# Performance work log

Hardware: AMD Instinct MI355X
Metric: run time of the kernel (lower is better)

The kernel has to match this reference:

```python
import jax, jax.numpy as jnp
import numpy as np

NUM_EMBEDDINGS = 512
EMBEDDING_DIM = 64
COMMITMENT_COST = 0.25


def setup_inputs() -> dict:
    key = jax.random.key(0)
    k1, k2 = jax.random.split(key)
    inputs = jax.random.normal(k1, (32, 4096, EMBEDDING_DIM), dtype=jnp.float32)
    # original init: uniform(-1/K, 1/K)
    weight = jax.random.uniform(
        k2, (NUM_EMBEDDINGS, EMBEDDING_DIM), dtype=jnp.float32,
        minval=-1.0 / NUM_EMBEDDINGS, maxval=1.0 / NUM_EMBEDDINGS)
    return {"inputs": inputs, "weight": weight, "is_training": 1}


def reference(inputs, weight, is_training):
    input_shape = inputs.shape
    flat = inputs.reshape(-1, EMBEDDING_DIM)                      # [N, D]
    distances = (jnp.sum(flat ** 2, axis=1, keepdims=True)
                 + jnp.sum(weight ** 2, axis=1)
                 - 2.0 * flat @ weight.T)                         # [N, K]
    encoding_indices = jnp.argmin(distances, axis=1)              # [N]
    # one-hot @ codebook == direct gather
    quantized = weight[encoding_indices].reshape(input_shape)

    sg = jax.lax.stop_gradient
    e_latent_loss = jnp.mean((sg(quantized) - inputs) ** 2)
    q_latent_loss = jnp.mean((quantized - sg(inputs)) ** 2)
    loss = q_latent_loss + COMMITMENT_COST * e_latent_loss

    quantized_st = inputs + sg(quantized - inputs)                # straight-through

    n = encoding_indices.shape[0]
    counts = jnp.zeros(NUM_EMBEDDINGS, dtype=jnp.float32).at[encoding_indices].add(1.0)
    avg_probs = counts / n
    perplexity = jnp.exp(-jnp.sum(avg_probs * jnp.log(avg_probs + 1e-10)))

    encoding_indices_show = encoding_indices.reshape(1, -1)
    return loss, quantized_st, perplexity, encoding_indices_show
```

## Files before the change

kernel.cpp:

```cpp
#include <hip/hip_runtime.h>

#define N_ROWS 131072
#define DIM 64
#define KCODES 512
#define MARGIN 1e-4f
#define QCAP 16384

typedef __attribute__((ext_vector_type(8))) short bf16x8;
typedef __attribute__((ext_vector_type(4))) float f32x4;


__device__ __forceinline__ float sqr_nf(float x) {
    float s = x * x;
    asm("" : "+v"(s));
    return s;
}

__device__ __forceinline__ unsigned short f2bf(float f) {
    unsigned u = __float_as_uint(f);
    u += 0x7fffu + ((u >> 16) & 1u);
    return (unsigned short)(u >> 16);
}
__device__ __forceinline__ float bf2f(unsigned short b) {
    return __uint_as_float(((unsigned)b) << 16);
}

__device__ __forceinline__ void cvtpair(float4 a, float4 b, bf16x8& hi, bf16x8& lo) {
    float v[8] = {a.x, a.y, a.z, a.w, b.x, b.y, b.z, b.w};
#pragma unroll
    for (int j = 0; j < 8; ++j) {
        unsigned short h = f2bf(v[j]);
        hi[j] = (short)h;
        lo[j] = (short)f2bf(v[j] - bf2f(h));
    }
}
__device__ __forceinline__ float4 scl(float4 v, float s) {
    return make_float4(v.x * s, v.y * s, v.z * s, v.w * s);
}

__global__ __launch_bounds__(256) void vq_wprep_k(
    const float* __restrict__ W, unsigned short* __restrict__ wfrag,
    float* __restrict__ bnp) {
    int code = blockIdx.x * 256 + threadIdx.x;
    float p[64];
#pragma unroll
    for (int i = 0; i < 16; ++i) {
        float4 v = reinterpret_cast<const float4*>(W)[code * 16 + i];
        p[i * 4 + 0] = v.x; p[i * 4 + 1] = v.y;
        p[i * 4 + 2] = v.z; p[i * 4 + 3] = v.w;
    }
    unsigned short hi[64], lo[64];
#pragma unroll
    for (int d = 0; d < 64; ++d) {
        hi[d] = f2bf(p[d]);
        lo[d] = f2bf(p[d] - bf2f(hi[d]));
    }
    {
        float r[8];
#pragma unroll
        for (int j = 0; j < 8; ++j) r[j] = sqr_nf(p[j]);
#pragma unroll
        for (int i = 1; i < 8; ++i)
#pragma unroll
            for (int j = 0; j < 8; ++j) r[j] += sqr_nf(p[i * 8 + j]);
        bnp[code] = ((r[0] + r[1]) + (r[2] + r[3])) + ((r[4] + r[5]) + (r[6] + r[7]));
    }
    const int cti = code >> 4, m = code & 15;
#pragma unroll
    for (int part = 0; part < 2; ++part) {
        const unsigned short* src = part ? lo : hi;
#pragma unroll
        for (int s = 0; s < 2; ++s) {
            int q = part * 2 + s;
#pragma unroll
            for (int kq = 0; kq < 4; ++kq) {
                int lane = kq * 16 + m;
                size_t off = ((size_t)(cti * 4 + q) * 64 + lane) * 8;
                *reinterpret_cast<uint4*>(wfrag + off) =
                    *reinterpret_cast<const uint4*>(src + s * 32 + kq * 8);
            }
        }
    }
}

__global__ __launch_bounds__(256, 4) void vq_score_k(
    const float* __restrict__ X, const unsigned short* __restrict__ wfrag,
    const float* __restrict__ bnp, float* __restrict__ out_idx) {
    const int tid = threadIdx.x;
    const int lane = tid & 63, w = tid >> 6;
    const int m = lane & 15, kq = lane >> 4;
    const long rbase = (long)blockIdx.x * 128;

    bf16x8 ahi[2][2], alo[2][2];
#pragma unroll
    for (int rt = 0; rt < 2; ++rt) {
        long row = rbase + w * 32 + rt * 16 + m;
        const float4* xp = reinterpret_cast<const float4*>(X + row * DIM);
        cvtpair(scl(xp[kq * 2], -2.f), scl(xp[kq * 2 + 1], -2.f),
                ahi[rt][0], alo[rt][0]);
        cvtpair(scl(xp[8 + kq * 2], -2.f), scl(xp[8 + kq * 2 + 1], -2.f),
                ahi[rt][1], alo[rt][1]);
    }

    float best[2][4], sec[2][4];
    int bidx[2][4];
#pragma unroll
    for (int rt = 0; rt < 2; ++rt)
#pragma unroll
        for (int j = 0; j < 4; ++j) { best[rt][j] = 3e38f; sec[rt][j] = 3e38f; bidx[rt][j] = 0; }

    const bf16x8* fb = reinterpret_cast<const bf16x8*>(wfrag);
    bf16x8 nb0 = fb[lane], nb1 = fb[64 + lane], nb2 = fb[128 + lane], nb3 = fb[192 + lane];
    for (int cti = 0; cti < 32; ++cti) {
        bf16x8 b0 = nb0, b1 = nb1, b2 = nb2, b3 = nb3;
        if (cti < 31) {
            int nbase = (cti + 1) * 256;
            nb0 = fb[nbase + lane];       nb1 = fb[nbase + 64 + lane];
            nb2 = fb[nbase + 128 + lane]; nb3 = fb[nbase + 192 + lane];
        }
        const int kk = cti * 16 + m;
        const float wn = bnp[kk];
        f32x4 c0 = {wn, wn, wn, wn};
        f32x4 c1 = {wn, wn, wn, wn};
        c0 = __builtin_amdgcn_mfma_f32_16x16x32_bf16(ahi[0][0], b0, c0, 0, 0, 0);
        c1 = __builtin_amdgcn_mfma_f32_16x16x32_bf16(ahi[1][0], b0, c1, 0, 0, 0);
        c0 = __builtin_amdgcn_mfma_f32_16x16x32_bf16(ahi[0][1], b1, c0, 0, 0, 0);
        c1 = __builtin_amdgcn_mfma_f32_16x16x32_bf16(ahi[1][1], b1, c1, 0, 0, 0);
        c0 = __builtin_amdgcn_mfma_f32_16x16x32_bf16(alo[0][0], b0, c0, 0, 0, 0);
        c1 = __builtin_amdgcn_mfma_f32_16x16x32_bf16(alo[1][0], b0, c1, 0, 0, 0);
        c0 = __builtin_amdgcn_mfma_f32_16x16x32_bf16(alo[0][1], b1, c0, 0, 0, 0);
        c1 = __builtin_amdgcn_mfma_f32_16x16x32_bf16(alo[1][1], b1, c1, 0, 0, 0);
        c0 = __builtin_amdgcn_mfma_f32_16x16x32_bf16(ahi[0][0], b2, c0, 0, 0, 0);
        c1 = __builtin_amdgcn_mfma_f32_16x16x32_bf16(ahi[1][0], b2, c1, 0, 0, 0);
        c0 = __builtin_amdgcn_mfma_f32_16x16x32_bf16(ahi[0][1], b3, c0, 0, 0, 0);
        c1 = __builtin_amdgcn_mfma_f32_16x16x32_bf16(ahi[1][1], b3, c1, 0, 0, 0);
#pragma unroll
        for (int rt = 0; rt < 2; ++rt)
#pragma unroll
            for (int j = 0; j < 4; ++j) {
                float s = (rt == 0) ? c0[j] : c1[j];
                float nb = fminf(best[rt][j], s);
                float ns = fminf(sec[rt][j], fmaxf(best[rt][j], s));
                bidx[rt][j] = (s < best[rt][j]) ? kk : bidx[rt][j];
                best[rt][j] = nb; sec[rt][j] = ns;
            }
    }

#pragma unroll
    for (int st = 1; st < 16; st <<= 1) {
#pragma unroll
        for (int rt = 0; rt < 2; ++rt)
#pragma unroll
            for (int j = 0; j < 4; ++j) {
                float ob = __shfl_xor(best[rt][j], st);
                float os = __shfl_xor(sec[rt][j], st);
                int oi = __shfl_xor(bidx[rt][j], st);
                if (ob < best[rt][j] || (ob == best[rt][j] && oi < bidx[rt][j])) {
                    sec[rt][j] = fminf(best[rt][j], os);
                    best[rt][j] = ob; bidx[rt][j] = oi;
                } else {
                    sec[rt][j] = fminf(sec[rt][j], ob);
                }
            }
    }

    if (m == 0) {
#pragma unroll
        for (int rt = 0; rt < 2; ++rt)
#pragma unroll
            for (int j = 0; j < 4; ++j) {
                int r = w * 32 + rt * 16 + kq * 4 + j;
                int id = (sec[rt][j] - best[rt][j] <= MARGIN) ? -1 : bidx[rt][j];
                out_idx[rbase + r] = (float)id;
            }
    }
}

__global__ __launch_bounds__(256, 4) void vq_post_k(
    const float* __restrict__ X, const float* __restrict__ Wf,
    const float* __restrict__ bnp,
    float* __restrict__ out_q, float* __restrict__ out_idx,
    unsigned* __restrict__ hist8, float* __restrict__ lossp,
    unsigned* __restrict__ qcount, unsigned* __restrict__ queue) {
    const int tid = threadIdx.x;
    const int lane = tid & 63, w = tid >> 6;
    const int g = lane >> 4, l16 = lane & 15;
    const long wbase = ((long)blockIdx.x * 4 + w) * 32;
    const unsigned hstripe = (blockIdx.x & 7) * KCODES;

    float idxv = (lane < 32) ? out_idx[wbase + lane] : 1.0f;

    int mypos = -1;
    if (lane < 32 && idxv < 0.f) {
        mypos = (int)atomicAdd(qcount, 1u);
        if (mypos < QCAP) queue[mypos] = (unsigned)(wbase + lane);
    }

    float4 xv[8], wv[8];
    int kk[8];
#pragma unroll
    for (int i = 0; i < 8; ++i) {
        int r = g * 8 + i;
        float kf = __shfl(idxv, r);
        kk[i] = (kf >= 0.f) ? (int)kf : -1;
        xv[i] = reinterpret_cast<const float4*>(X)[(wbase + r) * 16 + l16];
        int ksafe = (kk[i] >= 0) ? kk[i] : 0;
        wv[i] = reinterpret_cast<const float4*>(Wf)[(long)ksafe * 16 + l16];
    }

    float ls = 0.f;
#pragma unroll
    for (int i = 0; i < 8; ++i) {
        if (kk[i] >= 0) {
            float4 o; float t;
            t = wv[i].x - xv[i].x; o.x = xv[i].x + t; ls = fmaf(t, t, ls);
            t = wv[i].y - xv[i].y; o.y = xv[i].y + t; ls = fmaf(t, t, ls);
            t = wv[i].z - xv[i].z; o.z = xv[i].z + t; ls = fmaf(t, t, ls);
            t = wv[i].w - xv[i].w; o.w = xv[i].w + t; ls = fmaf(t, t, ls);
            reinterpret_cast<float4*>(out_q)[(wbase + g * 8 + i) * 16 + l16] = o;
            if (l16 == 0) atomicAdd(&hist8[hstripe + kk[i]], 1u);
        }
    }

    unsigned long long inl = __ballot(mypos >= QCAP);
    while (inl) {
        const int b = __ffsll((long long)inl) - 1;
        inl &= inl - 1;
        const long rrow = wbase + b;
        const float xvv = X[rrow * DIM + lane];
        float sq = sqr_nf(xvv);
        float rr = sq;
#pragma unroll
        for (int t2 = 1; t2 < 8; ++t2) rr += __shfl(sq, (lane & 7) + 8 * t2);
        float t01 = rr + __shfl_xor(rr, 1);
        float t03 = t01 + __shfl_xor(t01, 2);
        float Afull = t03 + __shfl_xor(t03, 4);
        const float A = __shfl(Afull, 0);
        float acc[8];
#pragma unroll
        for (int c = 0; c < 8; ++c) acc[c] = 0.f;
        for (int d0 = 0; d0 < 16; ++d0) {
            float x0 = __shfl(xvv, d0 * 4 + 0);
            float x1 = __shfl(xvv, d0 * 4 + 1);
            float x2 = __shfl(xvv, d0 * 4 + 2);
            float x3 = __shfl(xvv, d0 * 4 + 3);
#pragma unroll
            for (int c = 0; c < 8; ++c) {
                float4 wq = *reinterpret_cast<const float4*>(
                    &Wf[(lane * 8 + c) * DIM + d0 * 4]);
                acc[c] = fmaf(x0, wq.x, acc[c]);
                acc[c] = fmaf(x1, wq.y, acc[c]);
                acc[c] = fmaf(x2, wq.z, acc[c]);
                acc[c] = fmaf(x3, wq.w, acc[c]);
            }
        }
        float bs = 3e38f;
        int bi = 0;
#pragma unroll
        for (int c = 0; c < 8; ++c) {
            int kkk = lane * 8 + c;
            float u = A + bnp[kkk];
            float s2 = u - 2.0f * acc[c];
            if (s2 < bs) { bs = s2; bi = kkk; }
        }
#pragma unroll
        for (int st = 1; st < 64; st <<= 1) {
            float ob = __shfl_xor(bs, st);
            int oi = __shfl_xor(bi, st);
            if (ob < bs || (ob == bs && oi < bi)) { bs = ob; bi = oi; }
        }
        const int k = bi;
        if (lane == 0) {
            out_idx[rrow] = (float)k;
            atomicAdd(&hist8[hstripe + k], 1u);
        }
        float qv = Wf[k * DIM + lane];
        float diff = qv - xvv;
        out_q[rrow * DIM + lane] = xvv + diff;
        ls = fmaf(diff, diff, ls);
    }

#pragma unroll
    for (int st = 1; st < 64; st <<= 1) ls += __shfl_xor(ls, st);
    if (lane == 0 && ls != 0.f) atomicAdd(&lossp[blockIdx.x & 255], ls);
}

#define WTP 516
__global__ __launch_bounds__(1024) void vq_refine_k(
    const float* __restrict__ X, const float* __restrict__ Wf,
    const float* __restrict__ bnp,
    float* __restrict__ out_q, float* __restrict__ out_idx,
    unsigned* __restrict__ hist8, float* __restrict__ lossp,
    const unsigned* __restrict__ qcount, const unsigned* __restrict__ queue) {
    __shared__ float WT[64 * WTP];
    const int tid = threadIdx.x;
    const int lane = tid & 63, wv = tid >> 6;

#pragma unroll
    for (int i = 0; i < 8; ++i) {
        int f = i * 1024 + tid;
        int k = f >> 4, c4 = f & 15;
        float4 v = reinterpret_cast<const float4*>(Wf)[f];
        WT[(c4 * 4 + 0) * WTP + k] = v.x;
        WT[(c4 * 4 + 1) * WTP + k] = v.y;
        WT[(c4 * 4 + 2) * WTP + k] = v.z;
        WT[(c4 * 4 + 3) * WTP + k] = v.w;
    }
    __syncthreads();

    unsigned n = *qcount;
    if (n > QCAP) n = QCAP;
    const int gwave = blockIdx.x * 16 + wv;

    float ls = 0.f;
    for (unsigned j = gwave; j < n; j += 256 * 16) {
        const long row = (long)queue[j];
        const float xv = X[row * DIM + lane];
        float sq = sqr_nf(xv);
        float rr = sq;
#pragma unroll
        for (int t2 = 1; t2 < 8; ++t2) rr += __shfl(sq, (lane & 7) + 8 * t2);
        float t01 = rr + __shfl_xor(rr, 1);
        float t03 = t01 + __shfl_xor(t01, 2);
        float Afull = t03 + __shfl_xor(t03, 4);
        const float A = __shfl(Afull, 0);
        float acc[8];
#pragma unroll
        for (int c = 0; c < 8; ++c) acc[c] = 0.f;
        for (int d = 0; d < 64; ++d) {
            float xd = __shfl(xv, d);
#pragma unroll
            for (int c = 0; c < 8; ++c)
                acc[c] = fmaf(xd, WT[d * WTP + c * 64 + lane], acc[c]);
        }
        float bs = 3e38f;
        int bi = 0;
#pragma unroll
        for (int c = 0; c < 8; ++c) {
            int k = c * 64 + lane;
            float u = A + bnp[k];
            float s2 = u - 2.0f * acc[c];
            if (s2 < bs) { bs = s2; bi = k; }
        }
#pragma unroll
        for (int st = 1; st < 64; st <<= 1) {
            float ob = __shfl_xor(bs, st);
            int oi = __shfl_xor(bi, st);
            if (ob < bs || (ob == bs && oi < bi)) { bs = ob; bi = oi; }
        }
        const int k = bi;
        if (lane == 0) {
            out_idx[row] = (float)k;
            atomicAdd(&hist8[(j & 7) * KCODES + k], 1u);
        }
        float qv = WT[lane * WTP + k];
        float diff = qv - xv;
        out_q[row * DIM + lane] = xv + diff;
        ls = fmaf(diff, diff, ls);
    }

#pragma unroll
    for (int st = 1; st < 64; st <<= 1) ls += __shfl_xor(ls, st);
    if (lane == 0 && ls != 0.f) atomicAdd(&lossp[gwave & 255], ls);
}

__global__ __launch_bounds__(512) void vq_finalize_k(
    const unsigned* __restrict__ hist8, const float* __restrict__ lossp,
    float* __restrict__ out_loss, float* __restrict__ out_perp) {
    __shared__ float red[512];
    int t = threadIdx.x;
    unsigned c = 0;
#pragma unroll
    for (int s = 0; s < 8; ++s) c += hist8[s * KCODES + t];
    float p = (float)c * (1.0f / (float)N_ROWS);
    red[t] = p * logf(p + 1e-10f);
    __syncthreads();
    for (int off = 256; off; off >>= 1) {
        if (t < off) red[t] += red[t + off];
        __syncthreads();
    }
    if (t == 0) *out_perp = expf(-red[0]);
    __syncthreads();
    red[t] = (t < 256) ? lossp[t] : 0.f;
    __syncthreads();
    for (int off = 256; off; off >>= 1) {
        if (t < off) red[t] += red[t + off];
        __syncthreads();
    }
    if (t == 0) {
        float m = red[0] / (float)(N_ROWS * DIM);
        *out_loss = m + 0.25f * m;
    }
}

extern "C" void kernel_launch(void* const* d_in, const int* in_sizes, int n_in,
                              void* d_out, int out_size, void* d_ws, size_t ws_size,
                              hipStream_t stream) {
    const float* X = (const float*)d_in[0];
    const float* Wf = (const float*)d_in[1];

    float* out = (float*)d_out;
    float* out_loss = out;
    float* out_q = out + 1;
    float* out_perp = out + 1 + (long)N_ROWS * DIM;
    float* out_idx = out + 2 + (long)N_ROWS * DIM;

    unsigned* wsu = (unsigned*)d_ws;
    float* lossp = (float*)d_ws;
    unsigned* hist8 = wsu + 256;
    unsigned* qcount = wsu + 4352;
    unsigned* queue = wsu + 4360;
    float* bnp = (float*)(wsu + 20744);
    unsigned short* wfrag = (unsigned short*)(wsu + 21256);

    hipMemsetAsync(d_ws, 0, 17412, stream);
    vq_wprep_k<<<2, 256, 0, stream>>>(Wf, wfrag, bnp);
    vq_score_k<<<N_ROWS / 128, 256, 0, stream>>>(X, wfrag, bnp, out_idx);
    vq_post_k<<<N_ROWS / 128, 256, 0, stream>>>(X, Wf, bnp, out_q, out_idx,
                                                hist8, lossp, qcount, queue);
    vq_refine_k<<<256, 1024, 0, stream>>>(X, Wf, bnp, out_q, out_idx,
                                          hist8, lossp, qcount, queue);
    vq_finalize_k<<<1, 512, 0, stream>>>(hist8, lossp, out_loss, out_perp);
}
```

Baseline: 110.4 us.

## Halve rows per wave in score kernel and split MFMA accumulators into independent chains

The score kernel now handles 16 rows per wave instead of 32, which doubles the grid and raises the launch-bounds occupancy hint from 4 to 6. The six MFMAs per code tile are spread across three independent accumulators (hi*hi, lo*hi, hi*lo) that are summed at the end, instead of two long dependent chains. This aims to cut register pressure, raise occupancy and shorten MFMA dependency chains. In exchange, each codebook fragment loaded is reused across half as many rows, and the extra vector adds may change rounding of the scores slightly.

```diff
diff --git a/kernel.cpp b/kernel.cpp
--- a/kernel.cpp
+++ b/kernel.cpp
@@ -83,31 +83,26 @@
     }
 }
 
-__global__ __launch_bounds__(256, 4) void vq_score_k(
+__global__ __launch_bounds__(256, 6) void vq_score_k(
     const float* __restrict__ X, const unsigned short* __restrict__ wfrag,
     const float* __restrict__ bnp, float* __restrict__ out_idx) {
     const int tid = threadIdx.x;
     const int lane = tid & 63, w = tid >> 6;
     const int m = lane & 15, kq = lane >> 4;
-    const long rbase = (long)blockIdx.x * 128;
-
-    bf16x8 ahi[2][2], alo[2][2];
-#pragma unroll
-    for (int rt = 0; rt < 2; ++rt) {
-        long row = rbase + w * 32 + rt * 16 + m;
+    const long rbase = (long)blockIdx.x * 64;
+
+    bf16x8 ahi[2], alo[2];
+    {
+        long row = rbase + w * 16 + m;
         const float4* xp = reinterpret_cast<const float4*>(X + row * DIM);
-        cvtpair(scl(xp[kq * 2], -2.f), scl(xp[kq * 2 + 1], -2.f),
-                ahi[rt][0], alo[rt][0]);
-        cvtpair(scl(xp[8 + kq * 2], -2.f), scl(xp[8 + kq * 2 + 1], -2.f),
-                ahi[rt][1], alo[rt][1]);
-    }
-
-    float best[2][4], sec[2][4];
-    int bidx[2][4];
-#pragma unroll
-    for (int rt = 0; rt < 2; ++rt)
-#pragma unroll
-        for (int j = 0; j < 4; ++j) { best[rt][j] = 3e38f; sec[rt][j] = 3e38f; bidx[rt][j] = 0; }
+        cvtpair(scl(xp[kq * 2], -2.f), scl(xp[kq * 2 + 1], -2.f), ahi[0], alo[0]);
+        cvtpair(scl(xp[8 + kq * 2], -2.f), scl(xp[8 + kq * 2 + 1], -2.f), ahi[1], alo[1]);
+    }
+
+    float best[4], sec[4];
+    int bidx[4];
+#pragma unroll
+    for (int j = 0; j < 4; ++j) { best[j] = 3e38f; sec[j] = 3e38f; bidx[j] = 0; }
 
     const bf16x8* fb = reinterpret_cast<const bf16x8*>(wfrag);
     bf16x8 nb0 = fb[lane], nb1 = fb[64 + lane], nb2 = fb[128 + lane], nb3 = fb[192 + lane];
@@ -120,59 +115,49 @@
         }
         const int kk = cti * 16 + m;
         const float wn = bnp[kk];
-        f32x4 c0 = {wn, wn, wn, wn};
-        f32x4 c1 = {wn, wn, wn, wn};
-        c0 = __builtin_amdgcn_mfma_f32_16x16x32_bf16(ahi[0][0], b0, c0, 0, 0, 0);
-        c1 = __builtin_amdgcn_mfma_f32_16x16x32_bf16(ahi[1][0], b0, c1, 0, 0, 0);
-        c0 = __builtin_amdgcn_mfma_f32_16x16x32_bf16(ahi[0][1], b1, c0, 0, 0, 0);
-        c1 = __builtin_amdgcn_mfma_f32_16x16x32_bf16(ahi[1][1], b1, c1, 0, 0, 0);
-        c0 = __builtin_amdgcn_mfma_f32_16x16x32_bf16(alo[0][0], b0, c0, 0, 0, 0);
-        c1 = __builtin_amdgcn_mfma_f32_16x16x32_bf16(alo[1][0], b0, c1, 0, 0, 0);
-        c0 = __builtin_amdgcn_mfma_f32_16x16x32_bf16(alo[0][1], b1, c0, 0, 0, 0);
-        c1 = __builtin_amdgcn_mfma_f32_16x16x32_bf16(alo[1][1], b1, c1, 0, 0, 0);
-        c0 = __builtin_amdgcn_mfma_f32_16x16x32_bf16(ahi[0][0], b2, c0, 0, 0, 0);
-        c1 = __builtin_amdgcn_mfma_f32_16x16x32_bf16(ahi[1][0], b2, c1, 0, 0, 0);
-        c0 = __builtin_amdgcn_mfma_f32_16x16x32_bf16(ahi[0][1], b3, c0, 0, 0, 0);
-        c1 = __builtin_amdgcn_mfma_f32_16x16x32_bf16(ahi[1][1], b3, c1, 0, 0, 0);
-#pragma unroll
-        for (int rt = 0; rt < 2; ++rt)
-#pragma unroll
-            for (int j = 0; j < 4; ++j) {
-                float s = (rt == 0) ? c0[j] : c1[j];
-                float nb = fminf(best[rt][j], s);
-                float ns = fminf(sec[rt][j], fmaxf(best[rt][j], s));
-                bidx[rt][j] = (s < best[rt][j]) ? kk : bidx[rt][j];
-                best[rt][j] = nb; sec[rt][j] = ns;
+        f32x4 chh = {wn, wn, wn, wn};
+        f32x4 clh = {0.f, 0.f, 0.f, 0.f};
+        f32x4 chl = {0.f, 0.f, 0.f, 0.f};
+        chh = __builtin_amdgcn_mfma_f32_16x16x32_bf16(ahi[0], b0, chh, 0, 0, 0);
+        clh = __builtin_amdgcn_mfma_f32_16x16x32_bf16(alo[0], b0, clh, 0, 0, 0);
+        chl = __builtin_amdgcn_mfma_f32_16x16x32_bf16(ahi[0], b2, chl, 0, 0, 0);
+        chh = __builtin_amdgcn_mfma_f32_16x16x32_bf16(ahi[1], b1, chh, 0, 0, 0);
+        clh = __builtin_amdgcn_mfma_f32_16x16x32_bf16(alo[1], b1, clh, 0, 0, 0);
+        chl = __builtin_amdgcn_mfma_f32_16x16x32_bf16(ahi[1], b3, chl, 0, 0, 0);
+        f32x4 acc = (chh + clh) + chl;
+#pragma unroll
+        for (int j = 0; j < 4; ++j) {
+            float s = acc[j];
+            float nb = fminf(best[j], s);
+            float ns = fminf(sec[j], fmaxf(best[j], s));
+            bidx[j] = (s < best[j]) ? kk : bidx[j];
+            best[j] = nb; sec[j] = ns;
+        }
+    }
+
+#pragma unroll
+    for (int st = 1; st < 16; st <<= 1) {
+#pragma unroll
+        for (int j = 0; j < 4; ++j) {
+            float ob = __shfl_xor(best[j], st);
+            float os = __shfl_xor(sec[j], st);
+            int oi = __shfl_xor(bidx[j], st);
+            if (ob < best[j] || (ob == best[j] && oi < bidx[j])) {
+                sec[j] = fminf(best[j], os);
+                best[j] = ob; bidx[j] = oi;
+            } else {
+                sec[j] = fminf(sec[j], ob);
             }
-    }
-
-#pragma unroll
-    for (int st = 1; st < 16; st <<= 1) {
-#pragma unroll
-        for (int rt = 0; rt < 2; ++rt)
-#pragma unroll
-            for (int j = 0; j < 4; ++j) {
-                float ob = __shfl_xor(best[rt][j], st);
-                float os = __shfl_xor(sec[rt][j], st);
-                int oi = __shfl_xor(bidx[rt][j], st);
-                if (ob < best[rt][j] || (ob == best[rt][j] && oi < bidx[rt][j])) {
-                    sec[rt][j] = fminf(best[rt][j], os);
-                    best[rt][j] = ob; bidx[rt][j] = oi;
-                } else {
-                    sec[rt][j] = fminf(sec[rt][j], ob);
-                }
-            }
+        }
     }
 
     if (m == 0) {
 #pragma unroll
-        for (int rt = 0; rt < 2; ++rt)
-#pragma unroll
-            for (int j = 0; j < 4; ++j) {
-                int r = w * 32 + rt * 16 + kq * 4 + j;
-                int id = (sec[rt][j] - best[rt][j] <= MARGIN) ? -1 : bidx[rt][j];
-                out_idx[rbase + r] = (float)id;
-            }
+        for (int j = 0; j < 4; ++j) {
+            int r = w * 16 + kq * 4 + j;
+            int id = (sec[j] - best[j] <= MARGIN) ? -1 : bidx[j];
+            out_idx[rbase + r] = (float)id;
+        }
     }
 }
 
@@ -415,7 +400,7 @@
 
     hipMemsetAsync(d_ws, 0, 17412, stream);
     vq_wprep_k<<<2, 256, 0, stream>>>(Wf, wfrag, bnp);
-    vq_score_k<<<N_ROWS / 128, 256, 0, stream>>>(X, wfrag, bnp, out_idx);
+    vq_score_k<<<N_ROWS / 64, 256, 0, stream>>>(X, wfrag, bnp, out_idx);
     vq_post_k<<<N_ROWS / 128, 256, 0, stream>>>(X, Wf, bnp, out_q, out_idx,
                                                 hist8, lossp, qcount, queue);
     vq_refine_k<<<256, 1024, 0, stream>>>(X, Wf, bnp, out_q, out_idx,
```

Result: slower. 117.5 us (+6.5%).

## Double-buffer codebook fragment prefetch and stage code norms in shared memory

Applied to the files above, without the earlier changes.

The codebook fragment loads move from a one-tile-ahead prefetch to two interleaved register buffers that run two tiles ahead, hiding more global-load latency. Code norms are staged into LDS once per block instead of being read from global memory every iteration. MFMA chains are reordered per row tile into two independent accumulators (c0 and c1) that are summed afterwards, which shortens the dependent MFMA chain. The cost is more live registers for the second prefetch buffer, a block-wide barrier, and a changed summation order that may perturb near-tie argmin results.

```diff
diff --git a/kernel.cpp b/kernel.cpp
--- a/kernel.cpp
+++ b/kernel.cpp
@@ -83,13 +83,43 @@
     }
 }
 
+#define SCORE_STEP(CTI, B0, B1, B2, B3)                                           \
+    {                                                                             \
+        const int kk = (CTI) * 16 + m;                                            \
+        const float wn = bnp_s[kk];                                               \
+        _Pragma("unroll")                                                         \
+        for (int rt = 0; rt < 2; ++rt) {                                          \
+            f32x4 c0 = {wn, wn, wn, wn};                                          \
+            f32x4 c1 = {0.f, 0.f, 0.f, 0.f};                                      \
+            c0 = __builtin_amdgcn_mfma_f32_16x16x32_bf16(ahi[rt][0], B0, c0, 0, 0, 0); \
+            c1 = __builtin_amdgcn_mfma_f32_16x16x32_bf16(ahi[rt][0], B2, c1, 0, 0, 0); \
+            c0 = __builtin_amdgcn_mfma_f32_16x16x32_bf16(alo[rt][0], B0, c0, 0, 0, 0); \
+            c1 = __builtin_amdgcn_mfma_f32_16x16x32_bf16(ahi[rt][1], B3, c1, 0, 0, 0); \
+            c0 = __builtin_amdgcn_mfma_f32_16x16x32_bf16(ahi[rt][1], B1, c0, 0, 0, 0); \
+            c0 = __builtin_amdgcn_mfma_f32_16x16x32_bf16(alo[rt][1], B1, c0, 0, 0, 0); \
+            f32x4 acc = c0 + c1;                                                  \
+            _Pragma("unroll")                                                     \
+            for (int j = 0; j < 4; ++j) {                                         \
+                float s = acc[j];                                                 \
+                float nb = fminf(best[rt][j], s);                                 \
+                float ns = fminf(sec[rt][j], fmaxf(best[rt][j], s));              \
+                bidx[rt][j] = (s < best[rt][j]) ? kk : bidx[rt][j];               \
+                best[rt][j] = nb; sec[rt][j] = ns;                                \
+            }                                                                     \
+        }                                                                         \
+    }
+
 __global__ __launch_bounds__(256, 4) void vq_score_k(
     const float* __restrict__ X, const unsigned short* __restrict__ wfrag,
     const float* __restrict__ bnp, float* __restrict__ out_idx) {
+    __shared__ float bnp_s[KCODES];
     const int tid = threadIdx.x;
     const int lane = tid & 63, w = tid >> 6;
     const int m = lane & 15, kq = lane >> 4;
     const long rbase = (long)blockIdx.x * 128;
+
+    bnp_s[tid] = bnp[tid];
+    bnp_s[256 + tid] = bnp[256 + tid];
 
     bf16x8 ahi[2][2], alo[2][2];
 #pragma unroll
@@ -101,6 +131,7 @@
         cvtpair(scl(xp[8 + kq * 2], -2.f), scl(xp[8 + kq * 2 + 1], -2.f),
                 ahi[rt][1], alo[rt][1]);
     }
+    __syncthreads();
 
     float best[2][4], sec[2][4];
     int bidx[2][4];
@@ -110,40 +141,28 @@
         for (int j = 0; j < 4; ++j) { best[rt][j] = 3e38f; sec[rt][j] = 3e38f; bidx[rt][j] = 0; }
 
     const bf16x8* fb = reinterpret_cast<const bf16x8*>(wfrag);
-    bf16x8 nb0 = fb[lane], nb1 = fb[64 + lane], nb2 = fb[128 + lane], nb3 = fb[192 + lane];
-    for (int cti = 0; cti < 32; ++cti) {
-        bf16x8 b0 = nb0, b1 = nb1, b2 = nb2, b3 = nb3;
-        if (cti < 31) {
-            int nbase = (cti + 1) * 256;
-            nb0 = fb[nbase + lane];       nb1 = fb[nbase + 64 + lane];
-            nb2 = fb[nbase + 128 + lane]; nb3 = fb[nbase + 192 + lane];
-        }
-        const int kk = cti * 16 + m;
-        const float wn = bnp[kk];
-        f32x4 c0 = {wn, wn, wn, wn};
-        f32x4 c1 = {wn, wn, wn, wn};
-        c0 = __builtin_amdgcn_mfma_f32_16x16x32_bf16(ahi[0][0], b0, c0, 0, 0, 0);
-        c1 = __builtin_amdgcn_mfma_f32_16x16x32_bf16(ahi[1][0], b0, c1, 0, 0, 0);
-        c0 = __builtin_amdgcn_mfma_f32_16x16x32_bf16(ahi[0][1], b1, c0, 0, 0, 0);
-        c1 = __builtin_amdgcn_mfma_f32_16x16x32_bf16(ahi[1][1], b1, c1, 0, 0, 0);
-        c0 = __builtin_amdgcn_mfma_f32_16x16x32_bf16(alo[0][0], b0, c0, 0, 0, 0);
-        c1 = __builtin_amdgcn_mfma_f32_16x16x32_bf16(alo[1][0], b0, c1, 0, 0, 0);
-        c0 = __builtin_amdgcn_mfma_f32_16x16x32_bf16(alo[0][1], b1, c0, 0, 0, 0);
-        c1 = __builtin_amdgcn_mfma_f32_16x16x32_bf16(alo[1][1], b1, c1, 0, 0, 0);
-        c0 = __builtin_amdgcn_mfma_f32_16x16x32_bf16(ahi[0][0], b2, c0, 0, 0, 0);
-        c1 = __builtin_amdgcn_mfma_f32_16x16x32_bf16(ahi[1][0], b2, c1, 0, 0, 0);
-        c0 = __builtin_amdgcn_mfma_f32_16x16x32_bf16(ahi[0][1], b3, c0, 0, 0, 0);
-        c1 = __builtin_amdgcn_mfma_f32_16x16x32_bf16(ahi[1][1], b3, c1, 0, 0, 0);
-#pragma unroll
-        for (int rt = 0; rt < 2; ++rt)
-#pragma unroll
-            for (int j = 0; j < 4; ++j) {
-                float s = (rt == 0) ? c0[j] : c1[j];
-                float nb = fminf(best[rt][j], s);
-                float ns = fminf(sec[rt][j], fmaxf(best[rt][j], s));
-                bidx[rt][j] = (s < best[rt][j]) ? kk : bidx[rt][j];
-                best[rt][j] = nb; sec[rt][j] = ns;
-            }
+    bf16x8 pa0 = fb[lane], pa1 = fb[64 + lane], pa2 = fb[128 + lane], pa3 = fb[192 + lane];
+    bf16x8 pb0 = fb[256 + lane], pb1 = fb[320 + lane], pb2 = fb[384 + lane], pb3 = fb[448 + lane];
+
+    for (int cti = 0; cti < 32; cti += 2) {
+        {
+            bf16x8 b0 = pa0, b1 = pa1, b2 = pa2, b3 = pa3;
+            if (cti + 2 < 32) {
+                int nb = (cti + 2) * 256;
+                pa0 = fb[nb + lane];       pa1 = fb[nb + 64 + lane];
+                pa2 = fb[nb + 128 + lane]; pa3 = fb[nb + 192 + lane];
+            }
+            SCORE_STEP(cti, b0, b1, b2, b3);
+        }
+        {
+            bf16x8 b0 = pb0, b1 = pb1, b2 = pb2, b3 = pb3;
+            if (cti + 3 < 32) {
+                int nb = (cti + 3) * 256;
+                pb0 = fb[nb + lane];       pb1 = fb[nb + 64 + lane];
+                pb2 = fb[nb + 128 + lane]; pb3 = fb[nb + 192 + lane];
+            }
+            SCORE_STEP(cti + 1, b0, b1, b2, b3);
+        }
     }
 
 #pragma unroll
```

Result: slower. 148.2 us (+34.3%).

## Stage codebook fragments in LDS with 1024-thread score blocks

Applied to the files above, without the earlier changes.

The score kernel now uses 1024-thread blocks, each covering 512 rows. It copies the whole 128 KB bf16 codebook fragment array and the codeword norms into shared memory once per block, so the inner loop reads B operands from LDS rather than global/L2. The MFMA chain is also reordered into two independent accumulators per row tile, which are summed afterwards to shorten the dependency chain. In exchange, 128 KB of LDS per block caps occupancy at one block per CU, and launch_bounds(1024,4) may be unattainable and put pressure on registers.

```diff
diff --git a/kernel.cpp b/kernel.cpp
--- a/kernel.cpp
+++ b/kernel.cpp
@@ -83,13 +83,23 @@
     }
 }
 
-__global__ __launch_bounds__(256, 4) void vq_score_k(
+__global__ __launch_bounds__(1024, 4) void vq_score_k(
     const float* __restrict__ X, const unsigned short* __restrict__ wfrag,
     const float* __restrict__ bnp, float* __restrict__ out_idx) {
+    __shared__ __align__(16) unsigned short Wlds[65536];
+    __shared__ float bnp_s[KCODES];
     const int tid = threadIdx.x;
     const int lane = tid & 63, w = tid >> 6;
     const int m = lane & 15, kq = lane >> 4;
-    const long rbase = (long)blockIdx.x * 128;
+    const long rbase = (long)blockIdx.x * 512;
+
+    {
+        const uint4* g = reinterpret_cast<const uint4*>(wfrag);
+        uint4* l4 = reinterpret_cast<uint4*>(Wlds);
+#pragma unroll
+        for (int i = 0; i < 8; ++i) l4[i * 1024 + tid] = g[i * 1024 + tid];
+    }
+    if (tid < KCODES) bnp_s[tid] = bnp[tid];
 
     bf16x8 ahi[2][2], alo[2][2];
 #pragma unroll
@@ -101,6 +111,7 @@
         cvtpair(scl(xp[8 + kq * 2], -2.f), scl(xp[8 + kq * 2 + 1], -2.f),
                 ahi[rt][1], alo[rt][1]);
     }
+    __syncthreads();
 
     float best[2][4], sec[2][4];
     int bidx[2][4];
@@ -109,41 +120,37 @@
 #pragma unroll
         for (int j = 0; j < 4; ++j) { best[rt][j] = 3e38f; sec[rt][j] = 3e38f; bidx[rt][j] = 0; }
 
-    const bf16x8* fb = reinterpret_cast<const bf16x8*>(wfrag);
-    bf16x8 nb0 = fb[lane], nb1 = fb[64 + lane], nb2 = fb[128 + lane], nb3 = fb[192 + lane];
+    const bf16x8* fp = reinterpret_cast<const bf16x8*>(Wlds);
+    bf16x8 nb0 = fp[lane], nb1 = fp[64 + lane], nb2 = fp[128 + lane], nb3 = fp[192 + lane];
     for (int cti = 0; cti < 32; ++cti) {
         bf16x8 b0 = nb0, b1 = nb1, b2 = nb2, b3 = nb3;
         if (cti < 31) {
-            int nbase = (cti + 1) * 256;
-            nb0 = fb[nbase + lane];       nb1 = fb[nbase + 64 + lane];
-            nb2 = fb[nbase + 128 + lane]; nb3 = fb[nbase + 192 + lane];
+            int nbi = (cti + 1) * 256;
+            nb0 = fp[nbi + lane];       nb1 = fp[nbi + 64 + lane];
+            nb2 = fp[nbi + 128 + lane]; nb3 = fp[nbi + 192 + lane];
         }
         const int kk = cti * 16 + m;
-        const float wn = bnp[kk];
-        f32x4 c0 = {wn, wn, wn, wn};
-        f32x4 c1 = {wn, wn, wn, wn};
-        c0 = __builtin_amdgcn_mfma_f32_16x16x32_bf16(ahi[0][0], b0, c0, 0, 0, 0);
-        c1 = __builtin_amdgcn_mfma_f32_16x16x32_bf16(ahi[1][0], b0, c1, 0, 0, 0);
-        c0 = __builtin_amdgcn_mfma_f32_16x16x32_bf16(ahi[0][1], b1, c0, 0, 0, 0);
-        c1 = __builtin_amdgcn_mfma_f32_16x16x32_bf16(ahi[1][1], b1, c1, 0, 0, 0);
-        c0 = __builtin_amdgcn_mfma_f32_16x16x32_bf16(alo[0][0], b0, c0, 0, 0, 0);
-        c1 = __builtin_amdgcn_mfma_f32_16x16x32_bf16(alo[1][0], b0, c1, 0, 0, 0);
-        c0 = __builtin_amdgcn_mfma_f32_16x16x32_bf16(alo[0][1], b1, c0, 0, 0, 0);
-        c1 = __builtin_amdgcn_mfma_f32_16x16x32_bf16(alo[1][1], b1, c1, 0, 0, 0);
-        c0 = __builtin_amdgcn_mfma_f32_16x16x32_bf16(ahi[0][0], b2, c0, 0, 0, 0);
-        c1 = __builtin_amdgcn_mfma_f32_16x16x32_bf16(ahi[1][0], b2, c1, 0, 0, 0);
-        c0 = __builtin_amdgcn_mfma_f32_16x16x32_bf16(ahi[0][1], b3, c0, 0, 0, 0);
-        c1 = __builtin_amdgcn_mfma_f32_16x16x32_bf16(ahi[1][1], b3, c1, 0, 0, 0);
-#pragma unroll
-        for (int rt = 0; rt < 2; ++rt)
+        const float wn = bnp_s[kk];
+#pragma unroll
+        for (int rt = 0; rt < 2; ++rt) {
+            f32x4 c0 = {wn, wn, wn, wn};
+            f32x4 c1 = {0.f, 0.f, 0.f, 0.f};
+            c0 = __builtin_amdgcn_mfma_f32_16x16x32_bf16(ahi[rt][0], b0, c0, 0, 0, 0);
+            c1 = __builtin_amdgcn_mfma_f32_16x16x32_bf16(ahi[rt][0], b2, c1, 0, 0, 0);
+            c0 = __builtin_amdgcn_mfma_f32_16x16x32_bf16(alo[rt][0], b0, c0, 0, 0, 0);
+            c1 = __builtin_amdgcn_mfma_f32_16x16x32_bf16(ahi[rt][1], b3, c1, 0, 0, 0);
+            c0 = __builtin_amdgcn_mfma_f32_16x16x32_bf16(ahi[rt][1], b1, c0, 0, 0, 0);
+            c0 = __builtin_amdgcn_mfma_f32_16x16x32_bf16(alo[rt][1], b1, c0, 0, 0, 0);
+            f32x4 acc = c0 + c1;
 #pragma unroll
             for (int j = 0; j < 4; ++j) {
-                float s = (rt == 0) ? c0[j] : c1[j];
+                float s = acc[j];
                 float nb = fminf(best[rt][j], s);
                 float ns = fminf(sec[rt][j], fmaxf(best[rt][j], s));
                 bidx[rt][j] = (s < best[rt][j]) ? kk : bidx[rt][j];
                 best[rt][j] = nb; sec[rt][j] = ns;
             }
+        }
     }
 
 #pragma unroll
@@ -415,7 +422,7 @@
 
     hipMemsetAsync(d_ws, 0, 17412, stream);
     vq_wprep_k<<<2, 256, 0, stream>>>(Wf, wfrag, bnp);
-    vq_score_k<<<N_ROWS / 128, 256, 0, stream>>>(X, wfrag, bnp, out_idx);
+    vq_score_k<<<N_ROWS / 512, 1024, 0, stream>>>(X, wfrag, bnp, out_idx);
     vq_post_k<<<N_ROWS / 128, 256, 0, stream>>>(X, Wf, bnp, out_q, out_idx,
                                                 hist8, lossp, qcount, queue);
     vq_refine_k<<<256, 1024, 0, stream>>>(X, Wf, bnp, out_q, out_idx,
```

After: 112.2 us. No clear change (+1.7%).
